# Performance work log

Measured on AMD Instinct MI355X. Metric: run time of the kernel, lower is better.

## Reference

```python
import jax, jax.numpy as jnp
import numpy as np

EMBED_DIM = 1024
NUM_HEADS = 16
HEAD_DIM = EMBED_DIM // NUM_HEADS


def setup_inputs() -> dict:
    key = jax.random.key(0)
    ks = jax.random.split(key, 9)
    B, S, D = 2, 2048, EMBED_DIM
    scale = 1.0 / np.sqrt(D)
    x = jax.random.normal(ks[0], (B, S, D), dtype=jnp.float32)
    Wq = jax.random.normal(ks[1], (D, D), dtype=jnp.float32) * scale
    Wk = jax.random.normal(ks[2], (D, D), dtype=jnp.float32) * scale
    Wv = jax.random.normal(ks[3], (D, D), dtype=jnp.float32) * scale
    Wo = jax.random.normal(ks[4], (D, D), dtype=jnp.float32) * scale
    bq = jnp.zeros((D,), jnp.float32)
    bk = jnp.zeros((D,), jnp.float32)
    bv = jnp.zeros((D,), jnp.float32)
    bo = jnp.zeros((D,), jnp.float32)
    return {"x": x, "Wq": Wq, "bq": bq, "Wk": Wk, "bk": bk,
            "Wv": Wv, "bv": bv, "Wo": Wo, "bo": bo}


def reference(x, Wq, bq, Wk, bk, Wv, bv, Wo, bo):
    B, S, D = x.shape
    H, Dh = NUM_HEADS, HEAD_DIM
    # QKV projections -> [B, H, S, Dh]
    q = (x @ Wq + bq).reshape(B, S, H, Dh).transpose(0, 2, 1, 3)
    k = (x @ Wk + bk).reshape(B, S, H, Dh).transpose(0, 2, 1, 3)
    v = (x @ Wv + bv).reshape(B, S, H, Dh).transpose(0, 2, 1, 3)
    # scores [B, H, S, S], scaled by sqrt(head_dim)
    scores = jnp.einsum('bhqd,bhkd->bhqk', q, k) / jnp.sqrt(jnp.float32(Dh))
    attn = jax.nn.softmax(scores, axis=-1)
    out = jnp.einsum('bhqk,bhkd->bhqd', attn, v)  # [B, H, S, Dh]
    out = out.transpose(0, 2, 1, 3).reshape(B, S, D)
    return out @ Wo + bo
```

## Files before the change

kernel.cpp:

```cpp
#include <hip/hip_runtime.h>
#include <hip/hip_bf16.h>

typedef short bf16x8 __attribute__((ext_vector_type(8)));
typedef float f32x4 __attribute__((ext_vector_type(4)));
typedef float f32x16 __attribute__((ext_vector_type(16)));
typedef unsigned uint2v __attribute__((ext_vector_type(2)));
typedef unsigned uint4v __attribute__((ext_vector_type(4)));

#define MFMA16(a, b, c) __builtin_amdgcn_mfma_f32_16x16x32_bf16((a), (b), (c), 0, 0, 0)
#define MFMA32(a, b, c) __builtin_amdgcn_mfma_f32_32x32x16_bf16((a), (b), (c), 0, 0, 0)

#if __has_builtin(__builtin_amdgcn_exp2f)
#define EXP2(x) __builtin_amdgcn_exp2f(x)
#else
#define EXP2(x) exp2f(x)
#endif

static constexpr int B_ = 2, S_ = 2048, D_ = 1024, H_ = 16, DH = 64;
static constexpr int M_ = B_ * S_;
static constexpr int K_ = D_;
static constexpr float kQS = 0.18033688011112042f;

static __device__ __forceinline__ ushort f2bf(float f) {
    __hip_bfloat16 h = __float2bfloat16(f);
    return *reinterpret_cast<ushort*>(&h);
}
static __device__ __forceinline__ float bf2f(ushort u) {
    __hip_bfloat16 h;
    *reinterpret_cast<ushort*>(&h) = u;
    return __bfloat162float(h);
}

static __device__ __forceinline__ void gload16(const ushort* g, ushort* l) {
    __builtin_amdgcn_global_load_lds((const __attribute__((address_space(1))) void*)g,
                                     (__attribute__((address_space(3))) void*)l, 16, 0, 0);
}

static __device__ __forceinline__ unsigned pkbf(float lo, float hi) {
    return __builtin_amdgcn_perm(__builtin_bit_cast(unsigned, hi),
                                 __builtin_bit_cast(unsigned, lo), 0x07060302u);
}

__global__ __launch_bounds__(256) void prep5(const float* __restrict__ x,
                                             const float* __restrict__ W0,
                                             const float* __restrict__ W1,
                                             const float* __restrict__ W2,
                                             const float* __restrict__ W3,
                                             ushort* __restrict__ xb,
                                             ushort* __restrict__ T0,
                                             ushort* __restrict__ T1,
                                             ushort* __restrict__ T2,
                                             ushort* __restrict__ T3) {
    int z = blockIdx.z;
    int tx = threadIdx.x, ty = threadIdx.y;
    int t = ty * 32 + tx;
    if (z == 4) {
        int blk = blockIdx.y * 32 + blockIdx.x;
#pragma unroll
        for (int k = 0; k < 4; k++) {
            int i = blk * 1024 + k * 256 + t;
            float4 v = reinterpret_cast<const float4*>(x)[i];
            ushort4 o;
            o.x = f2bf(v.x); o.y = f2bf(v.y); o.z = f2bf(v.z); o.w = f2bf(v.w);
            reinterpret_cast<ushort4*>(xb)[i] = o;
        }
        return;
    }
    __shared__ float tile[32][33];
    const float* W = (z == 0) ? W0 : (z == 1) ? W1 : (z == 2) ? W2 : W3;
    ushort* T = (z == 0) ? T0 : (z == 1) ? T1 : (z == 2) ? T2 : T3;
    float sc = (z == 0) ? kQS : 1.0f;
    int bx = blockIdx.x, by = blockIdx.y;
#pragma unroll
    for (int i = 0; i < 4; i++)
        tile[ty + i * 8][tx] = W[(by * 32 + ty + i * 8) * D_ + bx * 32 + tx];
    __syncthreads();
#pragma unroll
    for (int i = 0; i < 4; i++)
        T[(bx * 32 + ty + i * 8) * K_ + by * 32 + tx] = f2bf(tile[tx][ty + i * 8] * sc);
}

template <int MODE, int TN>
__global__ __launch_bounds__(256, 3) void gemm128(const ushort* __restrict__ A,
                                                  const ushort* __restrict__ Wt,
                                                  const float* __restrict__ bias_q,
                                                  const float* __restrict__ bias_k,
                                                  const float* __restrict__ bias_v,
                                                  ushort* __restrict__ Qb,
                                                  ushort* __restrict__ Kb,
                                                  ushort* __restrict__ Vtb,
                                                  float* __restrict__ outf) {
    constexpr int NJ = TN / 32;
    __shared__ __align__(16) ushort As[128 * 32];
    __shared__ __align__(16) ushort Bs[TN * 32];

    int m0 = blockIdx.x * 128;
    int n0 = blockIdx.y * TN;
    int t = threadIdx.x;
    int lane = t & 63, w = t >> 6;
    int ln = lane & 15, lq = lane >> 4;
    int wm = (w >> 1) * 64, wn = (w & 1) * (TN / 2);

    int c0 = t, c1 = t + 256;
    const ushort* Ag0 = A + (size_t)(m0 + (c0 >> 2)) * K_ + (c0 & 3) * 8;
    const ushort* Ag1 = A + (size_t)(m0 + (c1 >> 2)) * K_ + (c1 & 3) * 8;
    const ushort* Bg0 = Wt + (size_t)(n0 + (c0 >> 2)) * K_ + (c0 & 3) * 8;
    const ushort* Bg1 = Wt + (size_t)(n0 + (c1 >> 2)) * K_ + (c1 & 3) * 8;
    ushort* Al0 = As + c0 * 8;
    ushort* Al1 = As + c1 * 8;
    ushort* Bl0 = Bs + c0 * 8;
    ushort* Bl1 = Bs + c1 * 8;

    const bool swp = (MODE == 1) || (n0 < 2048);

    f32x4 acc[4][NJ];
#pragma unroll
    for (int i = 0; i < 4; i++)
#pragma unroll
        for (int j = 0; j < NJ; j++) acc[i][j] = f32x4{0.f, 0.f, 0.f, 0.f};

    if (swp) {
        for (int k0 = 0; k0 < K_; k0 += 32) {
            gload16(Ag0 + k0, Al0);
            gload16(Ag1 + k0, Al1);
            gload16(Bg0 + k0, Bl0);
            if (TN == 128) gload16(Bg1 + k0, Bl1);
            __syncthreads();
            bf16x8 af[4], bfr[NJ];
#pragma unroll
            for (int i = 0; i < 4; i++)
                af[i] = *reinterpret_cast<const bf16x8*>(As + (wm + i * 16 + ln) * 32 + lq * 8);
#pragma unroll
            for (int j = 0; j < NJ; j++)
                bfr[j] = *reinterpret_cast<const bf16x8*>(Bs + (wn + j * 16 + ln) * 32 + lq * 8);
#pragma unroll
            for (int i = 0; i < 4; i++)
#pragma unroll
                for (int j = 0; j < NJ; j++)
                    acc[i][j] = MFMA16(bfr[j], af[i], acc[i][j]);
            __syncthreads();
        }
    } else {
        for (int k0 = 0; k0 < K_; k0 += 32) {
            gload16(Ag0 + k0, Al0);
            gload16(Ag1 + k0, Al1);
            gload16(Bg0 + k0, Bl0);
            if (TN == 128) gload16(Bg1 + k0, Bl1);
            __syncthreads();
            bf16x8 af[4], bfr[NJ];
#pragma unroll
            for (int i = 0; i < 4; i++)
                af[i] = *reinterpret_cast<const bf16x8*>(As + (wm + i * 16 + ln) * 32 + lq * 8);
#pragma unroll
            for (int j = 0; j < NJ; j++)
                bfr[j] = *reinterpret_cast<const bf16x8*>(Bs + (wn + j * 16 + ln) * 32 + lq * 8);
#pragma unroll
            for (int i = 0; i < 4; i++)
#pragma unroll
                for (int j = 0; j < NJ; j++)
                    acc[i][j] = MFMA16(af[i], bfr[j], acc[i][j]);
            __syncthreads();
        }
    }

    if (MODE == 1) {
#pragma unroll
        for (int j = 0; j < NJ; j++) {
            int nb = n0 + wn + j * 16 + lq * 4;
            float4 bv4 = *reinterpret_cast<const float4*>(bias_q + nb);
#pragma unroll
            for (int i = 0; i < 4; i++) {
                int m = m0 + wm + i * 16 + ln;
                float4 o;
                o.x = acc[i][j][0] + bv4.x;
                o.y = acc[i][j][1] + bv4.y;
                o.z = acc[i][j][2] + bv4.z;
                o.w = acc[i][j][3] + bv4.w;
                *reinterpret_cast<float4*>(outf + (size_t)m * D_ + nb) = o;
            }
        }
    } else if (n0 < 2048) {
        int which = n0 >> 10;
        const float* bp = which ? bias_k : bias_q;
        ushort* dst = which ? Kb : Qb;
        float bsc = which ? 1.0f : kQS;
#pragma unroll
        for (int j = 0; j < NJ; j++) {
            int nb = ((n0 + wn + j * 16) & 1023) + lq * 4;
            int h = nb >> 6, dhb = nb & 63;
            float4 bv4 = *reinterpret_cast<const float4*>(bp + nb);
            bv4.x *= bsc; bv4.y *= bsc; bv4.z *= bsc; bv4.w *= bsc;
#pragma unroll
            for (int i = 0; i < 4; i++) {
                int m = m0 + wm + i * 16 + ln;
                int b = m >> 11, s = m & 2047;
                ushort4 o4;
                o4.x = f2bf(acc[i][j][0] + bv4.x);
                o4.y = f2bf(acc[i][j][1] + bv4.y);
                o4.z = f2bf(acc[i][j][2] + bv4.z);
                o4.w = f2bf(acc[i][j][3] + bv4.w);
                *reinterpret_cast<ushort4*>(dst + (((size_t)(b * H_ + h) * S_) + s) * DH + dhb) = o4;
            }
        }
    } else {
#pragma unroll
        for (int j = 0; j < NJ; j++) {
            int n = n0 + wn + j * 16 + ln;
            int nn = n & 1023, h = nn >> 6, dh = nn & 63;
            float bv = bias_v[nn];
#pragma unroll
            for (int i = 0; i < 4; i++) {
                int m = m0 + wm + i * 16 + lq * 4;
                int b = m >> 11, s0 = m & 2047;
                ushort4 o4;
                o4.x = f2bf(acc[i][j][0] + bv);
                o4.y = f2bf(acc[i][j][1] + bv);
                o4.z = f2bf(acc[i][j][2] + bv);
                o4.w = f2bf(acc[i][j][3] + bv);
                *reinterpret_cast<ushort4*>(Vtb + (((size_t)(b * H_ + h) * DH) + dh) * S_ + s0) = o4;
            }
        }
    }
}

__global__ __launch_bounds__(256, 4) void attn32(const ushort* __restrict__ Q,
                                                 const ushort* __restrict__ K,
                                                 const ushort* __restrict__ Vt,
                                                 ushort* __restrict__ O1,
                                                 ushort* __restrict__ O2,
                                                 float* __restrict__ L) {
    __shared__ __align__(16) ushort Kl[2][4096];
    __shared__ __align__(16) ushort Vl[2][4096];

    int bid = blockIdx.x;
    int half = bid >> 9;
    int rem = bid & 511;
    int qb = rem & 15;
    int bh = rem >> 4;
    int t = threadIdx.x;
    int lane = t & 63, w = t >> 6;
    int ln = lane & 31, hi = lane >> 5;
    int q0 = qb * 128 + w * 32;

    const ushort* Qp = Q + (size_t)bh * S_ * DH;
    const ushort* Kp = K + (size_t)bh * S_ * DH + (size_t)half * 1024 * DH;
    const ushort* Vp = Vt + (size_t)bh * DH * S_ + (size_t)half * 1024;

    bf16x8 qf[4];
#pragma unroll
    for (int ks = 0; ks < 4; ks++)
        qf[ks] = *reinterpret_cast<const bf16x8*>(Qp + (size_t)(q0 + ln) * DH + ks * 16 + hi * 8);

    bf16x8 ones;
#pragma unroll
    for (int j = 0; j < 8; j++) ones[j] = (short)0x3F80;

    int c0 = t, c1 = t + 256;
    const ushort* Kg0 = Kp + (size_t)(c0 & 63) * DH + (c0 >> 6) * 8;
    const ushort* Kg1 = Kp + (size_t)(c1 & 63) * DH + (c1 >> 6) * 8;
    const ushort* Vg0 = Vp + (size_t)(c0 & 63) * S_ + (c0 >> 6) * 8;
    const ushort* Vg1 = Vp + (size_t)(c1 & 63) * S_ + (c1 >> 6) * 8;

    f32x16 o_acc[2];
    f32x16 l_acc;
#pragma unroll
    for (int r = 0; r < 16; r++) { o_acc[0][r] = 0.f; o_acc[1][r] = 0.f; l_acc[r] = 0.f; }

    gload16(Kg0, &Kl[0][c0 * 8]);
    gload16(Kg1, &Kl[0][c1 * 8]);
    gload16(Vg0, &Vl[0][c0 * 8]);
    gload16(Vg1, &Vl[0][c1 * 8]);

    for (int kt = 0; kt < 16; kt++) {
        int cur = kt & 1;
        __syncthreads();
        if (kt < 15) {
            int kb = (kt + 1) * 64;
            gload16(Kg0 + (size_t)kb * DH, &Kl[cur ^ 1][c0 * 8]);
            gload16(Kg1 + (size_t)kb * DH, &Kl[cur ^ 1][c1 * 8]);
            gload16(Vg0 + kb, &Vl[cur ^ 1][c0 * 8]);
            gload16(Vg1 + kb, &Vl[cur ^ 1][c1 * 8]);
        }
        const ushort* Kc = Kl[cur];
        const ushort* Vc = Vl[cur];
#pragma unroll
        for (int kb2 = 0; kb2 < 2; kb2++) {
            f32x16 sc;
#pragma unroll
            for (int r = 0; r < 16; r++) sc[r] = 0.f;
#pragma unroll
            for (int ks = 0; ks < 4; ks++) {
                bf16x8 kf = *reinterpret_cast<const bf16x8*>(
                    Kc + (ks * 2 + hi) * 512 + (kb2 * 32 + ln) * 8);
                sc = MFMA32(kf, qf[ks], sc);
            }
            unsigned pk[8];
#pragma unroll
            for (int j = 0; j < 8; j++)
                pk[j] = pkbf(EXP2(sc[2 * j]), EXP2(sc[2 * j + 1]));
            uint2v s0 = __builtin_amdgcn_permlane32_swap(pk[0], pk[2], false, false);
            uint2v s1 = __builtin_amdgcn_permlane32_swap(pk[1], pk[3], false, false);
            uint2v s2 = __builtin_amdgcn_permlane32_swap(pk[4], pk[6], false, false);
            uint2v s3 = __builtin_amdgcn_permlane32_swap(pk[5], pk[7], false, false);
            bf16x8 f0 = __builtin_bit_cast(bf16x8, (uint4v){s0.x, s1.x, s0.y, s1.y});
            bf16x8 f1 = __builtin_bit_cast(bf16x8, (uint4v){s2.x, s3.x, s2.y, s3.y});
            l_acc = MFMA32(f0, ones, l_acc);
            l_acc = MFMA32(f1, ones, l_acc);
#pragma unroll
            for (int h2 = 0; h2 < 2; h2++) {
                bf16x8 v0 = *reinterpret_cast<const bf16x8*>(
                    Vc + (kb2 * 4 + hi) * 512 + (h2 * 32 + ln) * 8);
                bf16x8 v1 = *reinterpret_cast<const bf16x8*>(
                    Vc + (kb2 * 4 + 2 + hi) * 512 + (h2 * 32 + ln) * 8);
                o_acc[h2] = MFMA32(f0, v0, o_acc[h2]);
                o_acc[h2] = MFMA32(f1, v1, o_acc[h2]);
            }
        }
    }

    ushort* Op = half ? O2 : O1;
    float* Lp = L + ((size_t)half * 32 + bh) * S_;
    int b = bh >> 4, h = bh & 15;
    if (ln == 0) {
#pragma unroll
        for (int r = 0; r < 16; r++)
            Lp[q0 + (r & 3) + 8 * (r >> 2) + 4 * hi] = l_acc[r];
    }
#pragma unroll
    for (int r = 0; r < 16; r++) {
        int s = q0 + (r & 3) + 8 * (r >> 2) + 4 * hi;
        float linv = 1.0f / l_acc[r];
        size_t base = (((size_t)(b * S_ + s)) * H_ + h) * DH;
        Op[base + ln] = f2bf(o_acc[0][r] * linv);
        Op[base + 32 + ln] = f2bf(o_acc[1][r] * linv);
    }
}

__global__ __launch_bounds__(256) void attn_comb(const ushort* __restrict__ O1,
                                                 const ushort* __restrict__ O2,
                                                 const float* __restrict__ L,
                                                 ushort* __restrict__ AO) {
    int i = blockIdx.x * 256 + threadIdx.x;
    int row = i >> 7;
    int col = (i & 127) * 8;
    int h = col >> 6;
    int b = row >> 11, s = row & 2047;
    int bh = b * 16 + h;
    float l1 = L[(size_t)bh * S_ + s];
    float l2 = L[((size_t)32 + bh) * S_ + s];
    float inv = 1.0f / (l1 + l2);
    float w1 = l1 * inv, w2 = l2 * inv;
    size_t off = (size_t)row * D_ + col;
    ushort4 a0 = reinterpret_cast<const ushort4*>(O1 + off)[0];
    ushort4 a1 = reinterpret_cast<const ushort4*>(O1 + off)[1];
    ushort4 b0 = reinterpret_cast<const ushort4*>(O2 + off)[0];
    ushort4 b1 = reinterpret_cast<const ushort4*>(O2 + off)[1];
    ushort4 o0, o1v;
    o0.x = f2bf(w1 * bf2f(a0.x) + w2 * bf2f(b0.x));
    o0.y = f2bf(w1 * bf2f(a0.y) + w2 * bf2f(b0.y));
    o0.z = f2bf(w1 * bf2f(a0.z) + w2 * bf2f(b0.z));
    o0.w = f2bf(w1 * bf2f(a0.w) + w2 * bf2f(b0.w));
    o1v.x = f2bf(w1 * bf2f(a1.x) + w2 * bf2f(b1.x));
    o1v.y = f2bf(w1 * bf2f(a1.y) + w2 * bf2f(b1.y));
    o1v.z = f2bf(w1 * bf2f(a1.z) + w2 * bf2f(b1.z));
    o1v.w = f2bf(w1 * bf2f(a1.w) + w2 * bf2f(b1.w));
    reinterpret_cast<ushort4*>(AO + off)[0] = o0;
    reinterpret_cast<ushort4*>(AO + off)[1] = o1v;
}

extern "C" void kernel_launch(void* const* d_in, const int* in_sizes, int n_in,
                              void* d_out, int out_size, void* d_ws, size_t ws_size,
                              hipStream_t stream) {
    const float* x  = (const float*)d_in[0];
    const float* Wq = (const float*)d_in[1];
    const float* bq = (const float*)d_in[2];
    const float* Wk = (const float*)d_in[3];
    const float* bk = (const float*)d_in[4];
    const float* Wv = (const float*)d_in[5];
    const float* bv = (const float*)d_in[6];
    const float* Wo = (const float*)d_in[7];
    const float* bo = (const float*)d_in[8];
    float* out = (float*)d_out;

    char* ws = (char*)d_ws;
    const size_t MB = 1024 * 1024;
    ushort* wtq = (ushort*)(ws + 0 * MB);
    ushort* wtk = (ushort*)(ws + 2 * MB);
    ushort* wtv = (ushort*)(ws + 4 * MB);
    ushort* wto = (ushort*)(ws + 6 * MB);
    ushort* xb  = (ushort*)(ws + 8 * MB);
    ushort* Qb  = (ushort*)(ws + 16 * MB);
    ushort* Kb  = (ushort*)(ws + 24 * MB);
    ushort* Vtb = (ushort*)(ws + 32 * MB);
    ushort* AO  = (ushort*)(ws + 40 * MB);
    ushort* O1  = (ushort*)(ws + 8 * MB);
    ushort* O2  = (ushort*)(ws + 48 * MB);
    float*  Lw  = (float*)(ws + 56 * MB);

    prep5<<<dim3(32, 32, 5), dim3(32, 8), 0, stream>>>(
        x, Wq, Wk, Wv, Wo, xb, wtq, wtk, wtv, wto);

    gemm128<0, 128><<<dim3(M_ / 128, 3072 / 128), 256, 0, stream>>>(
        xb, wtq, bq, bk, bv, Qb, Kb, Vtb, nullptr);

    attn32<<<1024, 256, 0, stream>>>(Qb, Kb, Vtb, O1, O2, Lw);
    attn_comb<<<(M_ * D_ / 8) / 256, 256, 0, stream>>>(O1, O2, Lw, AO);

    gemm128<1, 64><<<dim3(M_ / 128, D_ / 64), 256, 0, stream>>>(
        AO, wto, bo, nullptr, nullptr, nullptr, nullptr, nullptr, out);
}
```

Measured before the change: 197.6 us.

## Double GEMM K-tile to 64 with XOR-swizzled LDS and add MFMA setprio

The projection GEMM now stages 64-wide K slices per iteration instead of 32, which halves the number of barrier pairs. The LDS layout is XOR-swizzled by row so the wider rows avoid bank conflicts. The two duplicated swp loops are merged into one, with the branch moved inside. In the attention kernel, s_setprio raises wave priority around the MFMA bursts to interleave matrix and exp work across waves. LDS use doubles, which may reduce occupancy.

After: 224.0 us. 13.4% more time.

```diff
diff --git a/kernel.cpp b/kernel.cpp
--- a/kernel.cpp
+++ b/kernel.cpp
@@ -91,8 +91,9 @@
                                                   ushort* __restrict__ Vtb,
                                                   float* __restrict__ outf) {
     constexpr int NJ = TN / 32;
-    __shared__ __align__(16) ushort As[128 * 32];
-    __shared__ __align__(16) ushort Bs[TN * 32];
+    constexpr int BCH = TN * 64 / 8 / 256;
+    __shared__ __align__(16) ushort As[128 * 64];
+    __shared__ __align__(16) ushort Bs[TN * 64];
 
     int m0 = blockIdx.x * 128;
     int n0 = blockIdx.y * TN;
@@ -101,15 +102,24 @@
     int ln = lane & 15, lq = lane >> 4;
     int wm = (w >> 1) * 64, wn = (w & 1) * (TN / 2);
 
-    int c0 = t, c1 = t + 256;
-    const ushort* Ag0 = A + (size_t)(m0 + (c0 >> 2)) * K_ + (c0 & 3) * 8;
-    const ushort* Ag1 = A + (size_t)(m0 + (c1 >> 2)) * K_ + (c1 & 3) * 8;
-    const ushort* Bg0 = Wt + (size_t)(n0 + (c0 >> 2)) * K_ + (c0 & 3) * 8;
-    const ushort* Bg1 = Wt + (size_t)(n0 + (c1 >> 2)) * K_ + (c1 & 3) * 8;
-    ushort* Al0 = As + c0 * 8;
-    ushort* Al1 = As + c1 * 8;
-    ushort* Bl0 = Bs + c0 * 8;
-    ushort* Bl1 = Bs + c1 * 8;
+    const ushort* Ag[4];
+    ushort* Al[4];
+#pragma unroll
+    for (int q = 0; q < 4; q++) {
+        int c = t + q * 256;
+        int row = c >> 3, js = c & 7;
+        Ag[q] = A + (size_t)(m0 + row) * K_ + (js ^ (row & 7)) * 8;
+        Al[q] = As + c * 8;
+    }
+    const ushort* Bg[BCH];
+    ushort* Bl[BCH];
+#pragma unroll
+    for (int q = 0; q < BCH; q++) {
+        int c = t + q * 256;
+        int row = c >> 3, js = c & 7;
+        Bg[q] = Wt + (size_t)(n0 + row) * K_ + (js ^ (row & 7)) * 8;
+        Bl[q] = Bs + c * 8;
+    }
 
     const bool swp = (MODE == 1) || (n0 < 2048);
 
@@ -119,48 +129,38 @@
 #pragma unroll
         for (int j = 0; j < NJ; j++) acc[i][j] = f32x4{0.f, 0.f, 0.f, 0.f};
 
-    if (swp) {
-        for (int k0 = 0; k0 < K_; k0 += 32) {
-            gload16(Ag0 + k0, Al0);
-            gload16(Ag1 + k0, Al1);
-            gload16(Bg0 + k0, Bl0);
-            if (TN == 128) gload16(Bg1 + k0, Bl1);
-            __syncthreads();
+    for (int k0 = 0; k0 < K_; k0 += 64) {
+#pragma unroll
+        for (int q = 0; q < 4; q++) gload16(Ag[q] + k0, Al[q]);
+#pragma unroll
+        for (int q = 0; q < BCH; q++) gload16(Bg[q] + k0, Bl[q]);
+        __syncthreads();
+#pragma unroll
+        for (int kk = 0; kk < 2; kk++) {
             bf16x8 af[4], bfr[NJ];
 #pragma unroll
             for (int i = 0; i < 4; i++)
-                af[i] = *reinterpret_cast<const bf16x8*>(As + (wm + i * 16 + ln) * 32 + lq * 8);
+                af[i] = *reinterpret_cast<const bf16x8*>(
+                    As + (wm + i * 16 + ln) * 64 + ((kk * 4 + lq) ^ (ln & 7)) * 8);
 #pragma unroll
             for (int j = 0; j < NJ; j++)
-                bfr[j] = *reinterpret_cast<const bf16x8*>(Bs + (wn + j * 16 + ln) * 32 + lq * 8);
-#pragma unroll
-            for (int i = 0; i < 4; i++)
-#pragma unroll
-                for (int j = 0; j < NJ; j++)
-                    acc[i][j] = MFMA16(bfr[j], af[i], acc[i][j]);
-            __syncthreads();
-        }
-    } else {
-        for (int k0 = 0; k0 < K_; k0 += 32) {
-            gload16(Ag0 + k0, Al0);
-            gload16(Ag1 + k0, Al1);
-            gload16(Bg0 + k0, Bl0);
-            if (TN == 128) gload16(Bg1 + k0, Bl1);
-            __syncthreads();
-            bf16x8 af[4], bfr[NJ];
-#pragma unroll
-            for (int i = 0; i < 4; i++)
-                af[i] = *reinterpret_cast<const bf16x8*>(As + (wm + i * 16 + ln) * 32 + lq * 8);
-#pragma unroll
-            for (int j = 0; j < NJ; j++)
-                bfr[j] = *reinterpret_cast<const bf16x8*>(Bs + (wn + j * 16 + ln) * 32 + lq * 8);
-#pragma unroll
-            for (int i = 0; i < 4; i++)
-#pragma unroll
-                for (int j = 0; j < NJ; j++)
-                    acc[i][j] = MFMA16(af[i], bfr[j], acc[i][j]);
-            __syncthreads();
-        }
+                bfr[j] = *reinterpret_cast<const bf16x8*>(
+                    Bs + (wn + j * 16 + ln) * 64 + ((kk * 4 + lq) ^ (ln & 7)) * 8);
+            if (swp) {
+#pragma unroll
+                for (int i = 0; i < 4; i++)
+#pragma unroll
+                    for (int j = 0; j < NJ; j++)
+                        acc[i][j] = MFMA16(bfr[j], af[i], acc[i][j]);
+            } else {
+#pragma unroll
+                for (int i = 0; i < 4; i++)
+#pragma unroll
+                    for (int j = 0; j < NJ; j++)
+                        acc[i][j] = MFMA16(af[i], bfr[j], acc[i][j]);
+            }
+        }
+        __syncthreads();
     }
 
     if (MODE == 1) {
@@ -288,12 +288,14 @@
             f32x16 sc;
 #pragma unroll
             for (int r = 0; r < 16; r++) sc[r] = 0.f;
+            __builtin_amdgcn_s_setprio(1);
 #pragma unroll
             for (int ks = 0; ks < 4; ks++) {
                 bf16x8 kf = *reinterpret_cast<const bf16x8*>(
                     Kc + (ks * 2 + hi) * 512 + (kb2 * 32 + ln) * 8);
                 sc = MFMA32(kf, qf[ks], sc);
             }
+            __builtin_amdgcn_s_setprio(0);
             unsigned pk[8];
 #pragma unroll
             for (int j = 0; j < 8; j++)
@@ -304,6 +306,7 @@
             uint2v s3 = __builtin_amdgcn_permlane32_swap(pk[5], pk[7], false, false);
             bf16x8 f0 = __builtin_bit_cast(bf16x8, (uint4v){s0.x, s1.x, s0.y, s1.y});
             bf16x8 f1 = __builtin_bit_cast(bf16x8, (uint4v){s2.x, s3.x, s2.y, s3.y});
+            __builtin_amdgcn_s_setprio(1);
             l_acc = MFMA32(f0, ones, l_acc);
             l_acc = MFMA32(f1, ones, l_acc);
 #pragma unroll
@@ -315,6 +318,7 @@
                 o_acc[h2] = MFMA32(f0, v0, o_acc[h2]);
                 o_acc[h2] = MFMA32(f1, v1, o_acc[h2]);
             }
+            __builtin_amdgcn_s_setprio(0);
         }
     }
 
```

## Double-buffer GEMM shared-memory tiles and remap attention block order

Applied to the files above, without the earlier changes.

The projection GEMM now uses two shared-memory buffers for the A and B tiles. The next k-tile load is issued before the current tile's MFMAs, and one barrier per iteration replaces two, so global-to-LDS traffic can overlap compute. The swp branch moves inside the loop. Separately, the attention kernel permutes block indices (p&7)*128+(p>>3), likely to spread work across XCDs or improve K/V cache locality. Doubling LDS per block may reduce occupancy.

Result: slower. 212.5 us (+7.5%).

```diff
diff --git a/kernel.cpp b/kernel.cpp
--- a/kernel.cpp
+++ b/kernel.cpp
@@ -91,8 +91,8 @@
                                                   ushort* __restrict__ Vtb,
                                                   float* __restrict__ outf) {
     constexpr int NJ = TN / 32;
-    __shared__ __align__(16) ushort As[128 * 32];
-    __shared__ __align__(16) ushort Bs[TN * 32];
+    __shared__ __align__(16) ushort As[2][128 * 32];
+    __shared__ __align__(16) ushort Bs[2][TN * 32];
 
     int m0 = blockIdx.x * 128;
     int n0 = blockIdx.y * TN;
@@ -106,10 +106,6 @@
     const ushort* Ag1 = A + (size_t)(m0 + (c1 >> 2)) * K_ + (c1 & 3) * 8;
     const ushort* Bg0 = Wt + (size_t)(n0 + (c0 >> 2)) * K_ + (c0 & 3) * 8;
     const ushort* Bg1 = Wt + (size_t)(n0 + (c1 >> 2)) * K_ + (c1 & 3) * 8;
-    ushort* Al0 = As + c0 * 8;
-    ushort* Al1 = As + c1 * 8;
-    ushort* Bl0 = Bs + c0 * 8;
-    ushort* Bl1 = Bs + c1 * 8;
 
     const bool swp = (MODE == 1) || (n0 < 2048);
 
@@ -119,47 +115,42 @@
 #pragma unroll
         for (int j = 0; j < NJ; j++) acc[i][j] = f32x4{0.f, 0.f, 0.f, 0.f};
 
-    if (swp) {
-        for (int k0 = 0; k0 < K_; k0 += 32) {
-            gload16(Ag0 + k0, Al0);
-            gload16(Ag1 + k0, Al1);
-            gload16(Bg0 + k0, Bl0);
-            if (TN == 128) gload16(Bg1 + k0, Bl1);
-            __syncthreads();
-            bf16x8 af[4], bfr[NJ];
-#pragma unroll
-            for (int i = 0; i < 4; i++)
-                af[i] = *reinterpret_cast<const bf16x8*>(As + (wm + i * 16 + ln) * 32 + lq * 8);
-#pragma unroll
-            for (int j = 0; j < NJ; j++)
-                bfr[j] = *reinterpret_cast<const bf16x8*>(Bs + (wn + j * 16 + ln) * 32 + lq * 8);
+    gload16(Ag0, &As[0][c0 * 8]);
+    gload16(Ag1, &As[0][c1 * 8]);
+    gload16(Bg0, &Bs[0][c0 * 8]);
+    if (TN == 128) gload16(Bg1, &Bs[0][c1 * 8]);
+
+    for (int kt = 0; kt < 32; kt++) {
+        int cur = kt & 1;
+        __syncthreads();
+        if (kt < 31) {
+            int k0 = (kt + 1) * 32;
+            gload16(Ag0 + k0, &As[cur ^ 1][c0 * 8]);
+            gload16(Ag1 + k0, &As[cur ^ 1][c1 * 8]);
+            gload16(Bg0 + k0, &Bs[cur ^ 1][c0 * 8]);
+            if (TN == 128) gload16(Bg1 + k0, &Bs[cur ^ 1][c1 * 8]);
+        }
+        const ushort* Asc = As[cur];
+        const ushort* Bsc = Bs[cur];
+        bf16x8 af[4], bfr[NJ];
+#pragma unroll
+        for (int i = 0; i < 4; i++)
+            af[i] = *reinterpret_cast<const bf16x8*>(Asc + (wm + i * 16 + ln) * 32 + lq * 8);
+#pragma unroll
+        for (int j = 0; j < NJ; j++)
+            bfr[j] = *reinterpret_cast<const bf16x8*>(Bsc + (wn + j * 16 + ln) * 32 + lq * 8);
+        if (swp) {
 #pragma unroll
             for (int i = 0; i < 4; i++)
 #pragma unroll
                 for (int j = 0; j < NJ; j++)
                     acc[i][j] = MFMA16(bfr[j], af[i], acc[i][j]);
-            __syncthreads();
-        }
-    } else {
-        for (int k0 = 0; k0 < K_; k0 += 32) {
-            gload16(Ag0 + k0, Al0);
-            gload16(Ag1 + k0, Al1);
-            gload16(Bg0 + k0, Bl0);
-            if (TN == 128) gload16(Bg1 + k0, Bl1);
-            __syncthreads();
-            bf16x8 af[4], bfr[NJ];
-#pragma unroll
-            for (int i = 0; i < 4; i++)
-                af[i] = *reinterpret_cast<const bf16x8*>(As + (wm + i * 16 + ln) * 32 + lq * 8);
-#pragma unroll
-            for (int j = 0; j < NJ; j++)
-                bfr[j] = *reinterpret_cast<const bf16x8*>(Bs + (wn + j * 16 + ln) * 32 + lq * 8);
+        } else {
 #pragma unroll
             for (int i = 0; i < 4; i++)
 #pragma unroll
                 for (int j = 0; j < NJ; j++)
                     acc[i][j] = MFMA16(af[i], bfr[j], acc[i][j]);
-            __syncthreads();
         }
     }
 
@@ -232,7 +223,8 @@
     __shared__ __align__(16) ushort Kl[2][4096];
     __shared__ __align__(16) ushort Vl[2][4096];
 
-    int bid = blockIdx.x;
+    int p = blockIdx.x;
+    int bid = (p & 7) * 128 + (p >> 3);
     int half = bid >> 9;
     int rem = bid & 511;
     int qb = rem & 15;
```

## Read K/V fragments directly from global memory and remap block order for L2 reuse

Applied to the files above, without the earlier changes.

Drops the LDS double-buffered staging of K and V tiles and its per-iteration __syncthreads. Each lane now loads its MFMA operand fragments straight from global memory, relying on L2/cache reuse across the four waves and across blocks. Block IDs are also permuted so that consecutive hardware blocks are spread across groups, intended to improve locality or XCD distribution. This trades synchronisation and LDS traffic for redundant global loads with exposed latency and no explicit prefetch.

New measurement: 268.5 us. 35.9% more time.

```diff
diff --git a/kernel.cpp b/kernel.cpp
--- a/kernel.cpp
+++ b/kernel.cpp
@@ -229,10 +229,8 @@
                                                  ushort* __restrict__ O1,
                                                  ushort* __restrict__ O2,
                                                  float* __restrict__ L) {
-    __shared__ __align__(16) ushort Kl[2][4096];
-    __shared__ __align__(16) ushort Vl[2][4096];
-
-    int bid = blockIdx.x;
+    int p = blockIdx.x;
+    int bid = (p & 7) * 128 + (p >> 3);
     int half = bid >> 9;
     int rem = bid & 511;
     int qb = rem & 15;
@@ -255,43 +253,24 @@
 #pragma unroll
     for (int j = 0; j < 8; j++) ones[j] = (short)0x3F80;
 
-    int c0 = t, c1 = t + 256;
-    const ushort* Kg0 = Kp + (size_t)(c0 & 63) * DH + (c0 >> 6) * 8;
-    const ushort* Kg1 = Kp + (size_t)(c1 & 63) * DH + (c1 >> 6) * 8;
-    const ushort* Vg0 = Vp + (size_t)(c0 & 63) * S_ + (c0 >> 6) * 8;
-    const ushort* Vg1 = Vp + (size_t)(c1 & 63) * S_ + (c1 >> 6) * 8;
+    const ushort* Kb_lane = Kp + (size_t)ln * DH + hi * 8;
+    const ushort* Vb_lane = Vp + (size_t)ln * S_;
 
     f32x16 o_acc[2];
     f32x16 l_acc;
 #pragma unroll
     for (int r = 0; r < 16; r++) { o_acc[0][r] = 0.f; o_acc[1][r] = 0.f; l_acc[r] = 0.f; }
 
-    gload16(Kg0, &Kl[0][c0 * 8]);
-    gload16(Kg1, &Kl[0][c1 * 8]);
-    gload16(Vg0, &Vl[0][c0 * 8]);
-    gload16(Vg1, &Vl[0][c1 * 8]);
-
     for (int kt = 0; kt < 16; kt++) {
-        int cur = kt & 1;
-        __syncthreads();
-        if (kt < 15) {
-            int kb = (kt + 1) * 64;
-            gload16(Kg0 + (size_t)kb * DH, &Kl[cur ^ 1][c0 * 8]);
-            gload16(Kg1 + (size_t)kb * DH, &Kl[cur ^ 1][c1 * 8]);
-            gload16(Vg0 + kb, &Vl[cur ^ 1][c0 * 8]);
-            gload16(Vg1 + kb, &Vl[cur ^ 1][c1 * 8]);
-        }
-        const ushort* Kc = Kl[cur];
-        const ushort* Vc = Vl[cur];
 #pragma unroll
         for (int kb2 = 0; kb2 < 2; kb2++) {
+            const ushort* Kc = Kb_lane + (size_t)(kt * 64 + kb2 * 32) * DH;
             f32x16 sc;
 #pragma unroll
             for (int r = 0; r < 16; r++) sc[r] = 0.f;
 #pragma unroll
             for (int ks = 0; ks < 4; ks++) {
-                bf16x8 kf = *reinterpret_cast<const bf16x8*>(
-                    Kc + (ks * 2 + hi) * 512 + (kb2 * 32 + ln) * 8);
+                bf16x8 kf = *reinterpret_cast<const bf16x8*>(Kc + ks * 16);
                 sc = MFMA32(kf, qf[ks], sc);
             }
             unsigned pk[8];
@@ -308,10 +287,9 @@
             l_acc = MFMA32(f1, ones, l_acc);
 #pragma unroll
             for (int h2 = 0; h2 < 2; h2++) {
-                bf16x8 v0 = *reinterpret_cast<const bf16x8*>(
-                    Vc + (kb2 * 4 + hi) * 512 + (h2 * 32 + ln) * 8);
-                bf16x8 v1 = *reinterpret_cast<const bf16x8*>(
-                    Vc + (kb2 * 4 + 2 + hi) * 512 + (h2 * 32 + ln) * 8);
+                const ushort* Vc = Vb_lane + (size_t)h2 * 32 * S_ + kt * 64;
+                bf16x8 v0 = *reinterpret_cast<const bf16x8*>(Vc + (kb2 * 4 + hi) * 8);
+                bf16x8 v1 = *reinterpret_cast<const bf16x8*>(Vc + (kb2 * 4 + 2 + hi) * 8);
                 o_acc[h2] = MFMA32(f0, v0, o_acc[h2]);
                 o_acc[h2] = MFMA32(f1, v1, o_acc[h2]);
             }
```
